# Kernel optimization log

Measured on AMD Instinct MI355X. Metric: run time of the kernel, lower is better.

## Reference

```python
import jax, jax.numpy as jnp
import numpy as np

T, H, I, E, K = 8192, 1024, 2048, 8, 2


def setup_inputs() -> dict:
    key = jax.random.key(0)
    ks = jax.random.split(key, 6)
    s_h = 1.0 / np.sqrt(H)
    s_i = 1.0 / np.sqrt(I)
    return {
        "x": jax.random.normal(ks[0], (T, H), dtype=jnp.float32),
        "Wr": jax.random.normal(ks[1], (H, E), dtype=jnp.float32) * s_h,
        "br": jnp.zeros((E,), dtype=jnp.float32),
        "Wg": jax.random.normal(ks[2], (E, H, I), dtype=jnp.float32) * s_h,
        "Wu": jax.random.normal(ks[3], (E, H, I), dtype=jnp.float32) * s_h,
        "Wd": jax.random.normal(ks[4], (E, I, H), dtype=jnp.float32) * s_i,
    }


def reference(x, Wr, br, Wg, Wu, Wd):
    # Router: dense GEMM + top-k + sigmoid gate renormalization
    logits = x @ Wr + br                            # [T, E]
    topk_vals, topk_idx = jax.lax.top_k(logits, K)  # [T, K]
    g = jax.nn.sigmoid(topk_vals)
    g = g / (jnp.sum(g, axis=-1, keepdims=True) + 1e-10)
    # Scatter gates to dense [T, E] combine weights (zero for unselected experts)
    gates = jnp.zeros((x.shape[0], Wr.shape[1]), dtype=x.dtype)
    gates = gates.at[jnp.arange(x.shape[0])[:, None], topk_idx].add(g)
    # SwiGLU expert MLP, computed densely over experts and combined by gates
    h_gate = jnp.einsum("th,ehi->tei", x, Wg)       # [T, E, I]
    h_up = jnp.einsum("th,ehi->tei", x, Wu)
    h = jax.nn.silu(h_gate) * h_up
    h = h * gates[:, :, None]                       # fuse gate combine before down-proj
    out = jnp.einsum("tei,eih->th", h, Wd)          # [T, H]
    return out
```

## Files before the change

kernel.cpp:

```cpp
#include <hip/hip_runtime.h>
#include <hip/hip_bf16.h>
#include <stdint.h>

#define TT 8192
#define HH 1024
#define II 2048
#define EE 8
#define TOPK 2

typedef __bf16 bf16x8 __attribute__((ext_vector_type(8)));
typedef float f32x4 __attribute__((ext_vector_type(4)));

__device__ __forceinline__ unsigned short f2bf(float f) {
  union { float f; unsigned int u; } c; c.f = f;
  unsigned int u = c.u;
  u += 0x7FFFu + ((u >> 16) & 1u);
  return (unsigned short)(u >> 16);
}

__device__ __forceinline__ void gload_lds16(const void* g, void* l) {
  __builtin_amdgcn_global_load_lds((const __attribute__((address_space(1))) void*)g,
                                   (__attribute__((address_space(3))) void*)l, 16, 0, 0);
}

__global__ __launch_bounds__(256) void k_transpose_cvt(const float* __restrict__ src,
                                                       unsigned short* __restrict__ dst,
                                                       int R, int C) {
  __shared__ float tile[64][65];
  const float* s = src + (size_t)blockIdx.z * R * C;
  unsigned short* d = dst + (size_t)blockIdx.z * R * C;
  int r0 = blockIdx.y * 64, c0 = blockIdx.x * 64;
  int tx = threadIdx.x & 15;
  int ty = threadIdx.x >> 4;
#pragma unroll
  for (int i = 0; i < 4; ++i) {
    int rr = i * 16 + ty;
    float4 v = *reinterpret_cast<const float4*>(&s[(size_t)(r0 + rr) * C + c0 + tx * 4]);
    tile[rr][tx * 4 + 0] = v.x; tile[rr][tx * 4 + 1] = v.y;
    tile[rr][tx * 4 + 2] = v.z; tile[rr][tx * 4 + 3] = v.w;
  }
  __syncthreads();
#pragma unroll
  for (int i = 0; i < 4; ++i) {
    int cc = i * 16 + ty;
    ushort4 o;
    o.x = f2bf(tile[tx * 4 + 0][cc]);
    o.y = f2bf(tile[tx * 4 + 1][cc]);
    o.z = f2bf(tile[tx * 4 + 2][cc]);
    o.w = f2bf(tile[tx * 4 + 3][cc]);
    *reinterpret_cast<ushort4*>(&d[(size_t)(c0 + cc) * R + r0 + tx * 4]) = o;
  }
}

__global__ __launch_bounds__(256) void k_transpose_wgu(const float* __restrict__ src,
                                                       unsigned short* __restrict__ dst,
                                                       int mat) {
  __shared__ float tile[64][65];
  const float* s = src + (size_t)blockIdx.z * HH * II;
  unsigned short* d = dst + (size_t)blockIdx.z * 2 * II * HH;
  int r0 = blockIdx.y * 64, c0 = blockIdx.x * 64;
  int tx = threadIdx.x & 15;
  int ty = threadIdx.x >> 4;
#pragma unroll
  for (int i = 0; i < 4; ++i) {
    int rr = i * 16 + ty;
    float4 v = *reinterpret_cast<const float4*>(&s[(size_t)(r0 + rr) * II + c0 + tx * 4]);
    tile[rr][tx * 4 + 0] = v.x; tile[rr][tx * 4 + 1] = v.y;
    tile[rr][tx * 4 + 2] = v.z; tile[rr][tx * 4 + 3] = v.w;
  }
  __syncthreads();
#pragma unroll
  for (int i = 0; i < 4; ++i) {
    int cc = i * 16 + ty;
    int srow = c0 * 2 + ((cc >> 4) << 5) + mat * 16 + (cc & 15);
    ushort4 o;
    o.x = f2bf(tile[tx * 4 + 0][cc]);
    o.y = f2bf(tile[tx * 4 + 1][cc]);
    o.z = f2bf(tile[tx * 4 + 2][cc]);
    o.w = f2bf(tile[tx * 4 + 3][cc]);
    *reinterpret_cast<ushort4*>(&d[(size_t)srow * HH + r0 + tx * 4]) = o;
  }
}

__global__ __launch_bounds__(256) void k_router(const float* __restrict__ x,
                                                const float* __restrict__ Wr,
                                                const float* __restrict__ br,
                                                unsigned short* __restrict__ xb,
                                                int* __restrict__ tlist,
                                                float* __restrict__ glist,
                                                int* __restrict__ counts) {
  __shared__ float wrt[8][1024];
  __shared__ int lcount[8];
  __shared__ int lbase[8];
  __shared__ short ent_e[128];
  __shared__ short ent_slot[128];
  __shared__ float ent_g[128];
  int tid = threadIdx.x;
  for (int i = tid; i < 8192; i += 256) {
    wrt[i & 7][i >> 3] = Wr[i];
  }
  if (tid < 8) lcount[tid] = 0;
  __syncthreads();
  int w = tid >> 6, l = tid & 63;
  int t0 = blockIdx.x * 64;
  for (int it = 0; it < 16; ++it) {
    int t = t0 + w * 16 + it;
    const float4* xr = reinterpret_cast<const float4*>(x + (size_t)t * HH);
    float acc[8] = {0.f, 0.f, 0.f, 0.f, 0.f, 0.f, 0.f, 0.f};
#pragma unroll
    for (int j = 0; j < 4; ++j) {
      float4 xv = xr[j * 64 + l];
      int hbase = (j * 64 + l) * 4;
      ushort4 o;
      o.x = f2bf(xv.x); o.y = f2bf(xv.y); o.z = f2bf(xv.z); o.w = f2bf(xv.w);
      *reinterpret_cast<ushort4*>(xb + (size_t)t * HH + hbase) = o;
#pragma unroll
      for (int e = 0; e < 8; ++e) {
        float4 wv = *reinterpret_cast<const float4*>(&wrt[e][hbase]);
        acc[e] += xv.x * wv.x + xv.y * wv.y + xv.z * wv.z + xv.w * wv.w;
      }
    }
#pragma unroll
    for (int e = 0; e < 8; ++e)
#pragma unroll
      for (int off = 32; off > 0; off >>= 1) acc[e] += __shfl_xor(acc[e], off, 64);
    if (l == 0) {
      float lg[8];
#pragma unroll
      for (int e = 0; e < 8; ++e) lg[e] = acc[e] + br[e];
      int i0 = 0;
#pragma unroll
      for (int e = 1; e < 8; ++e) if (lg[e] > lg[i0]) i0 = e;
      int i1 = (i0 == 0) ? 1 : 0;
#pragma unroll
      for (int e = 0; e < 8; ++e) if (e != i0 && lg[e] > lg[i1]) i1 = e;
      float g0 = 1.f / (1.f + expf(-lg[i0]));
      float g1 = 1.f / (1.f + expf(-lg[i1]));
      float inv = 1.f / (g0 + g1 + 1e-10f);
      int idx = (w * 16 + it) * 2;
      int s0 = atomicAdd(&lcount[i0], 1);
      ent_e[idx] = (short)i0; ent_slot[idx] = (short)s0; ent_g[idx] = g0 * inv;
      int s1 = atomicAdd(&lcount[i1], 1);
      ent_e[idx + 1] = (short)i1; ent_slot[idx + 1] = (short)s1; ent_g[idx + 1] = g1 * inv;
    }
  }
  __syncthreads();
  if (tid < 8) lbase[tid] = atomicAdd(&counts[tid], lcount[tid]);
  __syncthreads();
  if (tid < 128) {
    int e = ent_e[tid];
    int slot = lbase[e] + ent_slot[tid];
    int t = t0 + (tid >> 1);
    tlist[e * TT + slot] = t;
    glist[e * TT + slot] = ent_g[tid];
  }
}

__global__ void k_offsets(const int* __restrict__ counts, int* __restrict__ offs) {
  if (threadIdx.x == 0) {
    int s = 0;
    for (int e = 0; e < EE; ++e) { offs[e] = s; s += counts[e]; }
  }
}

__global__ __launch_bounds__(256, 4) void k_gemm1(
    const unsigned short* __restrict__ xb,
    const unsigned short* __restrict__ WguT,
    const int* __restrict__ tlist, const float* __restrict__ glist,
    const int* __restrict__ counts, const int* __restrict__ offs,
    unsigned short* __restrict__ hbuf) {
  __shared__ unsigned short lsA[128 * 64];
  __shared__ unsigned short lsB[128 * 64];
  __shared__ int s_tok[128];
  __shared__ float s_gate[128];

  const int e = blockIdx.z;
  const int n_e = counts[e];
  const int row0 = blockIdx.y * 128;
  if (row0 >= n_e) return;
  const int n0 = blockIdx.x * 128;
  const int tid = threadIdx.x;

  if (tid < 128) {
    int r = row0 + tid;
    int tok = 0; float gt = 0.f;
    if (r < n_e) { tok = tlist[e * TT + r]; gt = glist[e * TT + r]; }
    s_tok[tid] = tok; s_gate[tid] = gt;
  }
  __syncthreads();

  const int scol = (tid & 7) ^ ((tid >> 3) & 7);
  const unsigned short* srcA[4];
  const unsigned short* srcB[4];
#pragma unroll
  for (int i = 0; i < 4; ++i) {
    int row = i * 32 + (tid >> 3);
    srcA[i] = xb + (size_t)s_tok[row] * HH + scol * 8;
    srcB[i] = WguT + ((size_t)e * 2 * II + n0 + row) * HH + scol * 8;
  }

  f32x4 zero = {0.f, 0.f, 0.f, 0.f};
  f32x4 acc[4][4];
#pragma unroll
  for (int m = 0; m < 4; ++m)
#pragma unroll
    for (int n = 0; n < 4; ++n) acc[m][n] = zero;

  const int l = tid & 63;
  const int w = tid >> 6;
  const int wr = (w >> 1) * 64;
  const int wc = (w & 1) * 64;
  const int lrow = l & 15;
  const int lk = l >> 4;
  const int swz = (l & 7) << 4;
  const int aoff0 = (wr + lrow) * 128 + lk * 16;
  const int boff0 = (wc + lrow) * 128 + lk * 16;
  const char* lcA = (const char*)lsA;
  const char* lcB = (const char*)lsB;

  for (int kt = 0; kt < HH / 64; ++kt) {
#pragma unroll
    for (int i = 0; i < 4; ++i) {
      gload_lds16(srcA[i] + kt * 64, (char*)lsA + i * 4096 + tid * 16);
      gload_lds16(srcB[i] + kt * 64, (char*)lsB + i * 4096 + tid * 16);
    }
    __syncthreads();
#pragma unroll
    for (int kk = 0; kk < 2; ++kk) {
      bf16x8 af[4], bf[4];
#pragma unroll
      for (int m = 0; m < 4; ++m)
        af[m] = *(const bf16x8*)(lcA + ((aoff0 + m * 2048 + kk * 64) ^ swz));
#pragma unroll
      for (int n = 0; n < 4; ++n)
        bf[n] = *(const bf16x8*)(lcB + ((boff0 + n * 2048 + kk * 64) ^ swz));
#pragma unroll
      for (int m = 0; m < 4; ++m)
#pragma unroll
        for (int n = 0; n < 4; ++n)
          acc[m][n] = __builtin_amdgcn_mfma_f32_16x16x32_bf16(af[m], bf[n], acc[m][n], 0, 0, 0);
    }
    __syncthreads();
  }

  const int obase = offs[e];
#pragma unroll
  for (int m = 0; m < 4; ++m)
#pragma unroll
    for (int n = 0; n < 4; n += 2)
#pragma unroll
      for (int r = 0; r < 4; ++r) {
        int rl = wr + m * 16 + lk * 4 + r;
        if (row0 + rl < n_e) {
          float gv = acc[m][n][r];
          float uv = acc[m][n + 1][r];
          float val = gv / (1.f + __expf(-gv)) * uv * s_gate[rl];
          int L = (n0 >> 1) + (wc >> 1) + (n >> 1) * 16 + lrow;
          hbuf[(size_t)(obase + row0 + rl) * II + L] = f2bf(val);
        }
      }
}

__global__ __launch_bounds__(256, 4) void k_gemm2(
    const unsigned short* __restrict__ hbuf,
    const unsigned short* __restrict__ WdT,
    const int* __restrict__ tlist,
    const int* __restrict__ counts, const int* __restrict__ offs,
    float* __restrict__ out) {
  __shared__ unsigned short lsA[128 * 64];
  __shared__ unsigned short lsB[128 * 64];
  __shared__ int s_tok[128];

  const int e = blockIdx.z;
  const int n_e = counts[e];
  const int row0 = blockIdx.y * 128;
  if (row0 >= n_e) return;
  const int n0 = blockIdx.x * 128;
  const int tid = threadIdx.x;
  const int obase = offs[e];

  if (tid < 128) {
    int r = row0 + tid;
    s_tok[tid] = (r < n_e) ? tlist[e * TT + r] : 0;
  }
  __syncthreads();

  const int scol = (tid & 7) ^ ((tid >> 3) & 7);
  const unsigned short* srcA[4];
  const unsigned short* srcB[4];
#pragma unroll
  for (int i = 0; i < 4; ++i) {
    int row = i * 32 + (tid >> 3);
    int ar = obase + row0 + row;
    if (ar > TT * TOPK - 1) ar = TT * TOPK - 1;
    srcA[i] = hbuf + (size_t)ar * II + scol * 8;
    srcB[i] = WdT + ((size_t)e * HH + n0 + row) * II + scol * 8;
  }

  f32x4 zero = {0.f, 0.f, 0.f, 0.f};
  f32x4 acc[4][4];
#pragma unroll
  for (int m = 0; m < 4; ++m)
#pragma unroll
    for (int n = 0; n < 4; ++n) acc[m][n] = zero;

  const int l = tid & 63;
  const int w = tid >> 6;
  const int wr = (w >> 1) * 64;
  const int wc = (w & 1) * 64;
  const int lrow = l & 15;
  const int lk = l >> 4;
  const int swz = (l & 7) << 4;
  const int aoff0 = (wr + lrow) * 128 + lk * 16;
  const int boff0 = (wc + lrow) * 128 + lk * 16;
  const char* lcA = (const char*)lsA;
  const char* lcB = (const char*)lsB;

  for (int kt = 0; kt < II / 64; ++kt) {
#pragma unroll
    for (int i = 0; i < 4; ++i) {
      gload_lds16(srcA[i] + kt * 64, (char*)lsA + i * 4096 + tid * 16);
      gload_lds16(srcB[i] + kt * 64, (char*)lsB + i * 4096 + tid * 16);
    }
    __syncthreads();
#pragma unroll
    for (int kk = 0; kk < 2; ++kk) {
      bf16x8 af[4], bf[4];
#pragma unroll
      for (int m = 0; m < 4; ++m)
        af[m] = *(const bf16x8*)(lcA + ((aoff0 + m * 2048 + kk * 64) ^ swz));
#pragma unroll
      for (int n = 0; n < 4; ++n)
        bf[n] = *(const bf16x8*)(lcB + ((boff0 + n * 2048 + kk * 64) ^ swz));
#pragma unroll
      for (int m = 0; m < 4; ++m)
#pragma unroll
        for (int n = 0; n < 4; ++n)
          acc[m][n] = __builtin_amdgcn_mfma_f32_16x16x32_bf16(af[m], bf[n], acc[m][n], 0, 0, 0);
    }
    __syncthreads();
  }

#pragma unroll
  for (int m = 0; m < 4; ++m)
#pragma unroll
    for (int n = 0; n < 4; ++n)
#pragma unroll
      for (int r = 0; r < 4; ++r) {
        int rl = wr + m * 16 + lk * 4 + r;
        if (row0 + rl < n_e) {
          int t = s_tok[rl];
          unsafeAtomicAdd(&out[(size_t)t * HH + n0 + wc + n * 16 + lrow], acc[m][n][r]);
        }
      }
}

extern "C" void kernel_launch(void* const* d_in, const int* in_sizes, int n_in,
                              void* d_out, int out_size, void* d_ws, size_t ws_size,
                              hipStream_t stream) {
  const float* x  = (const float*)d_in[0];
  const float* Wr = (const float*)d_in[1];
  const float* br = (const float*)d_in[2];
  const float* Wg = (const float*)d_in[3];
  const float* Wu = (const float*)d_in[4];
  const float* Wd = (const float*)d_in[5];
  float* out = (float*)d_out;

  char* ws = (char*)d_ws;
  size_t off = 0;
  auto alloc = [&](size_t bytes) {
    char* p = ws + off;
    off += (bytes + 255) & ~(size_t)255;
    return p;
  };
  unsigned short* xb   = (unsigned short*)alloc((size_t)TT * HH * 2);
  unsigned short* WguT = (unsigned short*)alloc((size_t)EE * 2 * II * HH * 2);
  unsigned short* WdT  = (unsigned short*)alloc((size_t)EE * HH * II * 2);
  unsigned short* hbuf = (unsigned short*)alloc((size_t)TT * TOPK * II * 2);
  int*   tlist  = (int*)alloc((size_t)EE * TT * 4);
  float* glist  = (float*)alloc((size_t)EE * TT * 4);
  int*   counts = (int*)alloc(128);
  int*   offs   = (int*)alloc(128);

  hipMemsetAsync(counts, 0, 128, stream);
  hipMemsetAsync(d_out, 0, (size_t)TT * HH * 4, stream);

  dim3 tgu(II / 64, HH / 64, EE);
  k_transpose_wgu<<<tgu, 256, 0, stream>>>(Wg, WguT, 0);
  k_transpose_wgu<<<tgu, 256, 0, stream>>>(Wu, WguT, 1);
  dim3 tg2(HH / 64, II / 64, EE);
  k_transpose_cvt<<<tg2, 256, 0, stream>>>(Wd, WdT, II, HH);

  k_router<<<TT / 64, 256, 0, stream>>>(x, Wr, br, xb, tlist, glist, counts);
  k_offsets<<<1, 64, 0, stream>>>(counts, offs);

  dim3 g1(2 * II / 128, TT / 128, EE);
  k_gemm1<<<g1, 256, 0, stream>>>(xb, WguT, tlist, glist, counts, offs, hbuf);
  dim3 g2(HH / 128, TT / 128, EE);
  k_gemm2<<<g2, 256, 0, stream>>>(hbuf, WdT, tlist, counts, offs, out);

  (void)in_sizes; (void)n_in; (void)out_size; (void)ws_size;
}
```

Before: 390.7 us.

## Restructure gate/up GEMM into 256x256 tiles with double-buffered LDS pipeline

The gate/up grouped GEMM now uses 256x256 output tiles with 512-thread blocks (8 waves, each owning a 128x64 sub-tile). It double-buffers A and B in LDS and interleaves async global-to-LDS prefetch of the next K slices with MFMA phases, using explicit vmcnt waits, s_barrier, sched_barrier and setprio. The aim is to hide global load latency behind compute and to raise arithmetic intensity per byte loaded. In exchange it needs 128KB of LDS and one block per CU, and experts whose token count is not a multiple of 256 waste more padded rows.

```diff
diff --git a/kernel.cpp b/kernel.cpp
--- a/kernel.cpp
+++ b/kernel.cpp
@@ -163,25 +163,58 @@
   }
 }
 
-__global__ __launch_bounds__(256, 4) void k_gemm1(
+#define READB(BP) do { _Pragma("unroll") \
+  for (int n = 0; n < 4; ++n) { \
+    bfr[2*n]   = *(const bf16x8*)((BP) + ((bbase + n*2048 + 0 ) ^ swz)); \
+    bfr[2*n+1] = *(const bf16x8*)((BP) + ((bbase + n*2048 + 64) ^ swz)); } } while(0)
+
+#define PHASE(AP, Q, STAGE_CODE, TAIL_CODE) do { \
+  bf16x8 af0 = *(const bf16x8*)((AP) + ((abase + (2*(Q))*2048 + 0 ) ^ swz)); \
+  bf16x8 af1 = *(const bf16x8*)((AP) + ((abase + (2*(Q))*2048 + 64) ^ swz)); \
+  bf16x8 af2 = *(const bf16x8*)((AP) + ((abase + (2*(Q)+1)*2048 + 0 ) ^ swz)); \
+  bf16x8 af3 = *(const bf16x8*)((AP) + ((abase + (2*(Q)+1)*2048 + 64) ^ swz)); \
+  STAGE_CODE; \
+  __builtin_amdgcn_sched_barrier(0); \
+  __builtin_amdgcn_s_barrier(); \
+  asm volatile("s_waitcnt lgkmcnt(0)" ::: "memory"); \
+  __builtin_amdgcn_sched_barrier(0); \
+  __builtin_amdgcn_s_setprio(1); \
+  _Pragma("unroll") \
+  for (int n = 0; n < 4; ++n) { \
+    acc[2*(Q)][n]   = __builtin_amdgcn_mfma_f32_16x16x32_bf16(af0, bfr[2*n],   acc[2*(Q)][n],   0,0,0); \
+    acc[2*(Q)][n]   = __builtin_amdgcn_mfma_f32_16x16x32_bf16(af1, bfr[2*n+1], acc[2*(Q)][n],   0,0,0); \
+    acc[2*(Q)+1][n] = __builtin_amdgcn_mfma_f32_16x16x32_bf16(af2, bfr[2*n],   acc[2*(Q)+1][n], 0,0,0); \
+    acc[2*(Q)+1][n] = __builtin_amdgcn_mfma_f32_16x16x32_bf16(af3, bfr[2*n+1], acc[2*(Q)+1][n], 0,0,0); \
+  } \
+  __builtin_amdgcn_s_setprio(0); \
+  TAIL_CODE; \
+  __builtin_amdgcn_sched_barrier(0); \
+  __builtin_amdgcn_s_barrier(); \
+  __builtin_amdgcn_sched_barrier(0); \
+} while(0)
+
+#define VM4() asm volatile("s_waitcnt vmcnt(4)" ::: "memory")
+#define VM0() asm volatile("s_waitcnt vmcnt(0)" ::: "memory")
+
+__global__ __launch_bounds__(512, 1) void k_gemm1(
     const unsigned short* __restrict__ xb,
     const unsigned short* __restrict__ WguT,
     const int* __restrict__ tlist, const float* __restrict__ glist,
     const int* __restrict__ counts, const int* __restrict__ offs,
     unsigned short* __restrict__ hbuf) {
-  __shared__ unsigned short lsA[128 * 64];
-  __shared__ unsigned short lsB[128 * 64];
-  __shared__ int s_tok[128];
-  __shared__ float s_gate[128];
+  __shared__ unsigned short lsA[2][2][128 * 64];
+  __shared__ unsigned short lsB[2][2][128 * 64];
+  __shared__ int s_tok[256];
+  __shared__ float s_gate[256];
 
   const int e = blockIdx.z;
   const int n_e = counts[e];
-  const int row0 = blockIdx.y * 128;
+  const int row0 = blockIdx.y * 256;
   if (row0 >= n_e) return;
-  const int n0 = blockIdx.x * 128;
+  const int n0 = blockIdx.x * 256;
   const int tid = threadIdx.x;
 
-  if (tid < 128) {
+  if (tid < 256) {
     int r = row0 + tid;
     int tok = 0; float gt = 0.f;
     if (r < n_e) { tok = tlist[e * TT + r]; gt = glist[e * TT + r]; }
@@ -189,73 +222,88 @@
   }
   __syncthreads();
 
-  const int scol = (tid & 7) ^ ((tid >> 3) & 7);
-  const unsigned short* srcA[4];
-  const unsigned short* srcB[4];
-#pragma unroll
-  for (int i = 0; i < 4; ++i) {
-    int row = i * 32 + (tid >> 3);
-    srcA[i] = xb + (size_t)s_tok[row] * HH + scol * 8;
-    srcB[i] = WguT + ((size_t)e * 2 * II + n0 + row) * HH + scol * 8;
-  }
-
-  f32x4 zero = {0.f, 0.f, 0.f, 0.f};
-  f32x4 acc[4][4];
-#pragma unroll
-  for (int m = 0; m < 4; ++m)
-#pragma unroll
-    for (int n = 0; n < 4; ++n) acc[m][n] = zero;
+  const int sr = tid >> 3;
+  const int sc = ((tid & 7) ^ (sr & 7)) * 8;
+  const unsigned short* sA[4];
+  const unsigned short* sB[4];
+#pragma unroll
+  for (int h = 0; h < 2; ++h)
+#pragma unroll
+    for (int j = 0; j < 2; ++j) {
+      sA[h * 2 + j] = xb + (size_t)s_tok[h * 128 + j * 64 + sr] * HH + sc;
+      sB[h * 2 + j] = WguT + ((size_t)e * 2 * II + n0 + h * 128 + j * 64 + sr) * HH + sc;
+    }
+
+  auto SA = [&](int d, int h, int kt) {
+    gload_lds16(sA[h * 2 + 0] + kt * 64, (char*)&lsA[d][h][0] + tid * 16);
+    gload_lds16(sA[h * 2 + 1] + kt * 64, (char*)&lsA[d][h][0] + 8192 + tid * 16);
+  };
+  auto SB = [&](int d, int h, int kt) {
+    gload_lds16(sB[h * 2 + 0] + kt * 64, (char*)&lsB[d][h][0] + tid * 16);
+    gload_lds16(sB[h * 2 + 1] + kt * 64, (char*)&lsB[d][h][0] + 8192 + tid * 16);
+  };
 
   const int l = tid & 63;
   const int w = tid >> 6;
-  const int wr = (w >> 1) * 64;
-  const int wc = (w & 1) * 64;
+  const int hA = w >> 2;
+  const int wcl = (w & 3) * 64;
+  const int cb = wcl & 127;
   const int lrow = l & 15;
   const int lk = l >> 4;
   const int swz = (l & 7) << 4;
-  const int aoff0 = (wr + lrow) * 128 + lk * 16;
-  const int boff0 = (wc + lrow) * 128 + lk * 16;
-  const char* lcA = (const char*)lsA;
-  const char* lcB = (const char*)lsB;
-
-  for (int kt = 0; kt < HH / 64; ++kt) {
-#pragma unroll
-    for (int i = 0; i < 4; ++i) {
-      gload_lds16(srcA[i] + kt * 64, (char*)lsA + i * 4096 + tid * 16);
-      gload_lds16(srcB[i] + kt * 64, (char*)lsB + i * 4096 + tid * 16);
-    }
-    __syncthreads();
-#pragma unroll
-    for (int kk = 0; kk < 2; ++kk) {
-      bf16x8 af[4], bf[4];
-#pragma unroll
-      for (int m = 0; m < 4; ++m)
-        af[m] = *(const bf16x8*)(lcA + ((aoff0 + m * 2048 + kk * 64) ^ swz));
-#pragma unroll
-      for (int n = 0; n < 4; ++n)
-        bf[n] = *(const bf16x8*)(lcB + ((boff0 + n * 2048 + kk * 64) ^ swz));
-#pragma unroll
-      for (int m = 0; m < 4; ++m)
-#pragma unroll
-        for (int n = 0; n < 4; ++n)
-          acc[m][n] = __builtin_amdgcn_mfma_f32_16x16x32_bf16(af[m], bf[n], acc[m][n], 0, 0, 0);
-    }
-    __syncthreads();
+  const int abase = lrow * 128 + lk * 16;
+  const int bbase = (cb + lrow) * 128 + lk * 16;
+  const char* a0 = (const char*)&lsA[0][hA][0];
+  const char* a1 = (const char*)&lsA[1][hA][0];
+  const char* b0 = (const char*)&lsB[0][wcl >> 7][0];
+  const char* b1 = (const char*)&lsB[1][wcl >> 7][0];
+
+  f32x4 zero = {0.f, 0.f, 0.f, 0.f};
+  f32x4 acc[8][4];
+#pragma unroll
+  for (int m = 0; m < 8; ++m)
+#pragma unroll
+    for (int n = 0; n < 4; ++n) acc[m][n] = zero;
+
+  SA(0, 0, 0); SA(0, 1, 0); SB(0, 0, 0); SB(0, 1, 0);
+  SB(1, 0, 1); SB(1, 1, 1);
+  VM4();
+  __builtin_amdgcn_sched_barrier(0);
+  __builtin_amdgcn_s_barrier();
+  __builtin_amdgcn_sched_barrier(0);
+
+  bf16x8 bfr[8];
+#pragma unroll 1
+  for (int it = 0; it < HH / 128; ++it) {
+    const bool pf = (it < HH / 128 - 1);
+    const int klo = 2 * it, khi = 2 * it + 1;
+
+    READB(b0);
+    PHASE(a0, 0, { SA(1, 0, khi); }, {});
+    PHASE(a0, 1, { SA(1, 1, khi); __builtin_amdgcn_sched_barrier(0);
+                   if (pf) SB(0, 0, klo + 2); }, {});
+    PHASE(a0, 2, { if (pf) SB(0, 1, klo + 2); }, {});
+    PHASE(a0, 3, {}, { if (pf) VM4(); else VM0(); });
+    READB(b1);
+    PHASE(a1, 0, { if (pf) SA(0, 0, klo + 2); }, {});
+    PHASE(a1, 1, { if (pf) SA(0, 1, klo + 2); }, {});
+    PHASE(a1, 2, { if (pf) SB(1, 0, khi + 2); }, {});
+    PHASE(a1, 3, { if (pf) SB(1, 1, khi + 2); }, { if (pf) VM4(); else VM0(); });
   }
 
   const int obase = offs[e];
 #pragma unroll
-  for (int m = 0; m < 4; ++m)
+  for (int m = 0; m < 8; ++m)
 #pragma unroll
     for (int n = 0; n < 4; n += 2)
 #pragma unroll
       for (int r = 0; r < 4; ++r) {
-        int rl = wr + m * 16 + lk * 4 + r;
+        int rl = hA * 128 + m * 16 + lk * 4 + r;
         if (row0 + rl < n_e) {
           float gv = acc[m][n][r];
           float uv = acc[m][n + 1][r];
           float val = gv / (1.f + __expf(-gv)) * uv * s_gate[rl];
-          int L = (n0 >> 1) + (wc >> 1) + (n >> 1) * 16 + lrow;
+          int L = ((n0 + wcl) >> 1) + (n >> 1) * 16 + lrow;
           hbuf[(size_t)(obase + row0 + rl) * II + L] = f2bf(val);
         }
       }
@@ -394,8 +442,8 @@
   k_router<<<TT / 64, 256, 0, stream>>>(x, Wr, br, xb, tlist, glist, counts);
   k_offsets<<<1, 64, 0, stream>>>(counts, offs);
 
-  dim3 g1(2 * II / 128, TT / 128, EE);
-  k_gemm1<<<g1, 256, 0, stream>>>(xb, WguT, tlist, glist, counts, offs, hbuf);
+  dim3 g1(2 * II / 256, TT / 256, EE);
+  k_gemm1<<<g1, 512, 0, stream>>>(xb, WguT, tlist, glist, counts, offs, hbuf);
   dim3 g2(HH / 128, TT / 128, EE);
   k_gemm2<<<g2, 256, 0, stream>>>(hbuf, WdT, tlist, counts, offs, out);
 
```

Measured after the change: 420.3 us. 7.6% more time.
